# Kernel tuning notes

Hardware: AMD Instinct MI355X
Metric: run time of the kernel (lower is better)

Reference implementation:

```python
import jax, jax.numpy as jnp
import numpy as np

N_SEG = 64        # number of graphs in batch
NEG_SLOPE = 0.2   # PyG GATConv leaky_relu slope


def seg_softmax(vals, seg, num_segments):
    # vals: [E, H]; softmax over entries sharing the same segment id
    m = jax.ops.segment_max(vals, seg, num_segments=num_segments)
    m = jnp.where(jnp.isfinite(m), m, 0.0)  # guard empty segments
    e = jnp.exp(vals - m[seg])
    s = jax.ops.segment_sum(e, seg, num_segments=num_segments)
    return e / (s[seg] + 1e-16)


def setup_inputs() -> dict:
    key = jax.random.key(0)
    ks = jax.random.split(key, 16)
    N, E, Fin, H, C1, C2 = 50000, 800000, 128, 4, 32, 128
    x = jax.random.normal(ks[0], (N, Fin), jnp.float32)
    edge_index = jax.random.randint(ks[1], (2, E), 0, N)
    batch = jnp.sort(jax.random.randint(ks[2], (N,), 0, N_SEG))
    sc = lambda fan: 1.0 / np.sqrt(fan)
    W_gat = jax.random.normal(ks[3], (Fin, H * C1), jnp.float32) * sc(Fin)
    att_src = jax.random.normal(ks[4], (H, C1), jnp.float32) * sc(C1)
    att_dst = jax.random.normal(ks[5], (H, C1), jnp.float32) * sc(C1)
    b_gat = jnp.zeros((H * C1,), jnp.float32)
    bn1_w = jax.random.uniform(ks[6], (H * C1,), jnp.float32, 0.5, 1.5)
    bn1_b = jax.random.normal(ks[7], (H * C1,), jnp.float32) * 0.1
    W_gcn = jax.random.normal(ks[8], (H * C1, C2), jnp.float32) * sc(H * C1)
    b_gcn = jnp.zeros((C2,), jnp.float32)
    bn2_w = jax.random.uniform(ks[9], (C2,), jnp.float32, 0.5, 1.5)
    bn2_b = jax.random.normal(ks[10], (C2,), jnp.float32) * 0.1
    W_gate = jax.random.normal(ks[11], (C2, 1), jnp.float32) * sc(C2)
    b_gate = jnp.zeros((1,), jnp.float32)
    W_fc = jax.random.normal(ks[12], (C2, 1), jnp.float32) * sc(C2)
    b_fc = jnp.zeros((1,), jnp.float32)
    return dict(x=x, edge_index=edge_index, batch=batch, W_gat=W_gat,
                att_src=att_src, att_dst=att_dst, b_gat=b_gat,
                bn1_w=bn1_w, bn1_b=bn1_b, W_gcn=W_gcn, b_gcn=b_gcn,
                bn2_w=bn2_w, bn2_b=bn2_b, W_gate=W_gate, b_gate=b_gate,
                W_fc=W_fc, b_fc=b_fc)


def reference(x, edge_index, batch, W_gat, att_src, att_dst, b_gat,
              bn1_w, bn1_b, W_gcn, b_gcn, bn2_w, bn2_b,
              W_gate, b_gate, W_fc, b_fc):
    N = x.shape[0]
    H, C1 = att_src.shape
    loops = jnp.arange(N)
    src = jnp.concatenate([edge_index[0], loops])  # message source j
    dst = jnp.concatenate([edge_index[1], loops])  # aggregation target i

    # ---- GATConv (heads=4, concat, add_self_loops) ----
    h = (x @ W_gat).reshape(N, H, C1)                       # [N,H,C1]
    a_src = jnp.einsum('nhc,hc->nh', h, att_src)
    a_dst = jnp.einsum('nhc,hc->nh', h, att_dst)
    e = jax.nn.leaky_relu(a_src[src] + a_dst[dst], NEG_SLOPE)  # [E',H]
    alpha = seg_softmax(e, dst, N)
    msg = h[src] * alpha[..., None]                          # [E',H,C1]
    out1 = jax.ops.segment_sum(msg, dst, num_segments=N).reshape(N, H * C1) + b_gat
    out1 = jax.nn.elu(out1)
    out1 = out1 * bn1_w + bn1_b          # BatchNorm1d (eval: mean 0, var 1)
    # dropout: identity (eval mode)

    # ---- GCNConv (self-loops, symmetric normalization) ----
    deg = jax.ops.segment_sum(jnp.ones_like(dst, dtype=x.dtype), dst, num_segments=N)
    dinv = jax.lax.rsqrt(jnp.maximum(deg, 1.0))
    norm = dinv[src] * dinv[dst]                             # [E']
    h2 = out1 @ W_gcn                                        # [N,C2]
    out2 = jax.ops.segment_sum(h2[src] * norm[:, None], dst, num_segments=N) + b_gcn
    out2 = jax.nn.elu(out2)
    out2 = out2 * bn2_w + bn2_b

    # ---- GlobalAttention pooling ----
    gate = out2 @ W_gate + b_gate                            # [N,1]
    w = seg_softmax(gate, batch, N_SEG)
    graph_rep = jax.ops.segment_sum(w * out2, batch, num_segments=N_SEG)  # [G,C2]

    out = graph_rep @ W_fc + b_fc                            # [G,1]
    return out.squeeze(1)
```

## Files before the change

### kernel.cpp

```cpp
#include <hip/hip_runtime.h>
#include <math.h>


#define NEG_SLOPE 0.2f
#define BKT_BITS 7
#define BKT_SIZE 128
#define CHUNK_A 4096

typedef __attribute__((ext_vector_type(8))) short short8v;
typedef __attribute__((ext_vector_type(4))) float floatx4;

__device__ __forceinline__ int lower_bound_i(const int* a, int n, int key) {
    int lo = 0, hi = n;
    while (lo < hi) {
        int mid = (lo + hi) >> 1;
        if (a[mid] < key) lo = mid + 1; else hi = mid;
    }
    return lo;
}

__device__ __forceinline__ unsigned pack_bf16(float lo, float hi) {
    unsigned ua = __float_as_uint(lo);
    unsigned ub = __float_as_uint(hi);
    ua = ua + 0x7fffu + ((ua >> 16) & 1u);
    ub = ub + 0x7fffu + ((ub >> 16) & 1u);
    return (ua >> 16) | (ub & 0xffff0000u);
}

__device__ __forceinline__ unsigned short bf16_1(float v) {
    unsigned u = __float_as_uint(v);
    u = u + 0x7fffu + ((u >> 16) & 1u);
    return (unsigned short)(u >> 16);
}

__global__ __launch_bounds__(256) void k_front(
    const float* __restrict__ W1, const float* __restrict__ atts,
    const float* __restrict__ attd, const float* __restrict__ W2,
    unsigned short* __restrict__ Wf1, unsigned short* __restrict__ Wf2,
    const int* __restrict__ dst, int* __restrict__ bcount, int E, int NB)
{
    const int b = blockIdx.x;
    if (b < 2) {
        const int NCT = b ? 8 : 9;
        const float* W = b ? W2 : W1;
        unsigned short* Wf = b ? Wf2 : Wf1;
        const int lim = NCT * 4 * 64 * 8;
        for (int idx = threadIdx.x; idx < lim; idx += 256) {
            int j = idx & 7;
            int lane = (idx >> 3) & 63;
            int frag = idx >> 9;
            int ct = frag >> 2, ks = frag & 3;
            int quad = lane >> 4, l16 = lane & 15;
            int k = ks * 32 + quad * 8 + j;
            float v;
            if (ct < 8) {
                v = W[k * 128 + ct * 16 + l16];
            } else if (l16 < 4) {
                float s = 0.f;
                for (int c = 0; c < 32; c++) s += W1[k * 128 + l16 * 32 + c] * atts[l16 * 32 + c];
                v = s;
            } else if (l16 < 8) {
                int h = l16 - 4;
                float s = 0.f;
                for (int c = 0; c < 32; c++) s += W1[k * 128 + h * 32 + c] * attd[h * 32 + c];
                v = s;
            } else v = 0.f;
            Wf[idx] = bf16_1(v);
        }
    } else {
        __shared__ int h[512];
        const int tid = threadIdx.x;
        for (int i = tid; i < 512; i += 256) h[i] = 0;
        __syncthreads();
        int base = (b - 2) * 2048;
#pragma unroll
        for (int k = 0; k < 8; k++) {
            int e = base + k * 256 + tid;
            if (e < E) atomicAdd(&h[dst[e] >> BKT_BITS], 1);
        }
        __syncthreads();
        for (int i = tid; i < NB; i += 256) {
            int c = h[i];
            if (c) atomicAdd(&bcount[i], c);
        }
    }
}

template<int MODE>
__global__ __launch_bounds__(256) void k_gemm_mfma(
    const void* __restrict__ Ain, const unsigned short* __restrict__ Wf,
    unsigned* __restrict__ Cb, int N,
    const float* __restrict__ dinv,
    float* __restrict__ aS, float* __restrict__ aD)
{
    constexpr int NCT = (MODE == 0) ? 9 : 8;
    const int tid = threadIdx.x;
    const int wv = tid >> 6, lane = tid & 63;
    const int quad = lane >> 4, l16 = lane & 15;
    const int n0 = blockIdx.x * 64;
    const int arow = n0 + wv * 16 + l16;
    const bool rowok = arow < N;

    floatx4 acc[NCT];
#pragma unroll
    for (int ct = 0; ct < NCT; ct++) acc[ct] = (floatx4){0.f, 0.f, 0.f, 0.f};

    union AV { unsigned u[4]; short8v v; };

#pragma unroll
    for (int ks = 0; ks < 4; ks++) {
        AV a;
        a.u[0] = a.u[1] = a.u[2] = a.u[3] = 0u;
        if (rowok) {
            if (MODE == 0) {
                const float* A = (const float*)Ain;
                const float* p = A + (size_t)arow * 128 + ks * 32 + quad * 8;
                float4 va = *(const float4*)(p);
                float4 vb = *(const float4*)(p + 4);
                a.u[0] = pack_bf16(va.x, va.y);
                a.u[1] = pack_bf16(va.z, va.w);
                a.u[2] = pack_bf16(vb.x, vb.y);
                a.u[3] = pack_bf16(vb.z, vb.w);
            } else {
                const unsigned short* A = (const unsigned short*)Ain;
                a.v = *(const short8v*)(A + (size_t)arow * 128 + ks * 32 + quad * 8);
            }
        }
#pragma unroll
        for (int ct = 0; ct < NCT; ct++) {
            short8v bv = *(const short8v*)(Wf + ((ct * 4 + ks) << 9) + lane * 8);
            acc[ct] = __builtin_amdgcn_mfma_f32_16x16x32_bf16(a.v, bv, acc[ct], 0, 0, 0);
        }
    }

#pragma unroll
    for (int r = 0; r < 4; r++) {
        int n = n0 + wv * 16 + quad * 4 + r;
        if (n >= N) continue;
        float s = MODE ? dinv[n] : 1.f;
#pragma unroll
        for (int ct = 0; ct < 4; ct++) {
            Cb[(size_t)n * 64 + ct * 16 + l16] =
                pack_bf16(acc[ct][r] * s, acc[ct + 4][r] * s);
        }
        if (MODE == 0) {
            float e = acc[8][r];
            if (l16 < 4) aS[(size_t)n * 4 + l16] = e;
            else if (l16 < 8) aD[(size_t)n * 4 + (l16 - 4)] = e;
        }
    }
}

__global__ __launch_bounds__(512) void k_bscan(const int* __restrict__ bcount,
                                               int* __restrict__ bb,
                                               int* __restrict__ bcur, int NB)
{
    __shared__ int sc[512];
    const int tid = threadIdx.x;
    int own = (tid < NB) ? bcount[tid] : 0;
    sc[tid] = own;
    __syncthreads();
    for (int st = 1; st < 512; st <<= 1) {
        int v = 0;
        if (tid >= st) v = sc[tid - st];
        __syncthreads();
        if (tid >= st) sc[tid] += v;
        __syncthreads();
    }
    int excl = sc[tid] - own;
    if (tid < NB) { bb[tid] = excl; bcur[tid] = excl; }
    if (tid == 511) { bb[NB] = sc[511]; bcur[NB] = sc[511]; }
}

__global__ __launch_bounds__(256) void k_binA(const int* __restrict__ ei,
                                              int* __restrict__ bcur,
                                              int2* __restrict__ pairs,
                                              int E, int NB)
{
    __shared__ int h[512];
    __shared__ int base[512];
    const int tid = threadIdx.x;
    for (int i = tid; i < NB + 1; i += 256) h[i] = 0;
    __syncthreads();
    const int c0 = blockIdx.x * CHUNK_A;
    int s[16], d[16], b[16];
#pragma unroll
    for (int k = 0; k < 16; k++) {
        int e = c0 + k * 256 + tid;
        bool v = e < E;
        s[k] = v ? ei[e] : 0;
        d[k] = v ? ei[E + e] : 0;
        b[k] = v ? (d[k] >> BKT_BITS) : NB;
        atomicAdd(&h[b[k]], 1);
    }
    __syncthreads();
    for (int i = tid; i < NB + 1; i += 256) {
        int c = h[i];
        base[i] = c ? atomicAdd(&bcur[i], c) : 0;
        h[i] = 0;
    }
    __syncthreads();
#pragma unroll
    for (int k = 0; k < 16; k++) {
        int r = atomicAdd(&h[b[k]], 1);
        pairs[base[b[k]] + r] = make_int2(s[k], d[k]);
    }
}

__global__ __launch_bounds__(256) void k_binB(const int2* __restrict__ pairs,
                                              const int* __restrict__ bb,
                                              int* __restrict__ csr,
                                              int* __restrict__ offs,
                                              float* __restrict__ dinv,
                                              int N, int NB, int E)
{
    __shared__ int hist[BKT_SIZE], start[BKT_SIZE], cur[BKT_SIZE];
    __shared__ int sc[BKT_SIZE];
    const int tid = threadIdx.x;
    const int b = blockIdx.x;
    const int d0 = b << BKT_BITS;
    const int pbg = bb[b], peg = bb[b + 1];

    if (tid < BKT_SIZE) { hist[tid] = 0; cur[tid] = 0; }
    __syncthreads();
    for (int i = pbg + tid; i < peg; i += 256)
        atomicAdd(&hist[pairs[i].y - d0], 1);
    __syncthreads();
    int own = (tid < BKT_SIZE) ? hist[tid] : 0;
    if (tid < BKT_SIZE) sc[tid] = own;
    __syncthreads();
    for (int st = 1; st < BKT_SIZE; st <<= 1) {
        int v = 0;
        bool act = (tid < BKT_SIZE) && (tid >= st);
        if (act) v = sc[tid - st];
        __syncthreads();
        if (act) sc[tid] += v;
        __syncthreads();
    }
    if (tid < BKT_SIZE) {
        int abs0 = pbg + (sc[tid] - own);
        start[tid] = abs0;
        int d = d0 + tid;
        if (d < N) {
            offs[d] = abs0;
            dinv[d] = rsqrtf((float)(own + 1));
        }
    }
    if (tid == 0 && b == NB - 1) offs[N] = E;
    __syncthreads();
    for (int i = pbg + tid; i < peg; i += 256) {
        int2 p = pairs[i];
        int ld = p.y - d0;
        int r = atomicAdd(&cur[ld], 1);
        csr[start[ld] + r] = p.x;
    }
}

__global__ __launch_bounds__(256) void k_gat_aggr(
    const unsigned* __restrict__ hb, const float* __restrict__ aSg,
    const float* __restrict__ aDg, const int* __restrict__ offs,
    const int* __restrict__ csr,
    const float* __restrict__ bgat, const float* __restrict__ bn1w,
    const float* __restrict__ bn1b,
    unsigned short* __restrict__ raw1b, int N)
{
    __shared__ __align__(16) float s_u[4][64][4];
    __shared__ int s_s[4][64];

    const int wid = threadIdx.x >> 6;
    const int lane = threadIdx.x & 63;
    const int n = blockIdx.x * 4 + wid;
    if (n >= N) return;

    const int beg = offs[n];
    const int cnt = offs[n + 1] - beg + 1;
    const float4 ad = *(const float4*)(aDg + (size_t)n * 4);
    const int hA = lane >> 5;
    const float* pu = &s_u[wid][0][2 * hA];
    const int* ps = &s_s[wid][0];

    float t0 = 0.f, t1 = 0.f, t2 = 0.f, t3 = 0.f;
    float accLo = 0.f, accHi = 0.f;

    for (int base = 0; base < cnt; base += 64) {
        int idx = base + lane;
        bool valid = idx < cnt;
        int src = n;
        if (valid && idx > 0) src = csr[beg + idx - 1];
        float u0 = 0.f, u1 = 0.f, u2 = 0.f, u3 = 0.f;
        if (valid) {
            float4 as = *(const float4*)(aSg + (size_t)src * 4);
            float l0 = as.x + ad.x; l0 = (l0 > 0.f) ? l0 : NEG_SLOPE * l0;
            float l1 = as.y + ad.y; l1 = (l1 > 0.f) ? l1 : NEG_SLOPE * l1;
            float l2 = as.z + ad.z; l2 = (l2 > 0.f) ? l2 : NEG_SLOPE * l2;
            float l3 = as.w + ad.w; l3 = (l3 > 0.f) ? l3 : NEG_SLOPE * l3;
            u0 = __expf(l0); u1 = __expf(l1); u2 = __expf(l2); u3 = __expf(l3);
        }
        t0 += u0; t1 += u1; t2 += u2; t3 += u3;
        s_s[wid][lane] = src;
        *(float4*)&s_u[wid][lane][0] = make_float4(u0, u2, u1, u3);

        int cc = min(64, cnt - base);
        int j = 0;
        for (; j + 8 <= cc; j += 8) {
            int sj[8]; float2 uj[8]; unsigned vv[8];
#pragma unroll
            for (int k = 0; k < 8; k++) sj[k] = ps[j + k];
#pragma unroll
            for (int k = 0; k < 8; k++) uj[k] = *(const float2*)&pu[(j + k) * 4];
#pragma unroll
            for (int k = 0; k < 8; k++) vv[k] = hb[sj[k] * 64 + lane];
#pragma unroll
            for (int k = 0; k < 8; k++) {
                float lo = __uint_as_float(vv[k] << 16);
                float hi = __uint_as_float(vv[k] & 0xffff0000u);
                accLo += uj[k].x * lo;
                accHi += uj[k].y * hi;
            }
        }
        for (; j < cc; j++) {
            int sj = ps[j];
            float2 uv = *(const float2*)&pu[j * 4];
            unsigned v = hb[sj * 64 + lane];
            accLo += uv.x * __uint_as_float(v << 16);
            accHi += uv.y * __uint_as_float(v & 0xffff0000u);
        }
    }
#pragma unroll
    for (int msk = 1; msk < 64; msk <<= 1) {
        t0 += __shfl_xor(t0, msk);
        t1 += __shfl_xor(t1, msk);
        t2 += __shfl_xor(t2, msk);
        t3 += __shfl_xor(t3, msk);
    }
    float sLo = (hA ? t1 : t0) + 1e-16f;
    float sHi = (hA ? t3 : t2) + 1e-16f;
    float o0 = accLo / sLo + bgat[lane];
    o0 = (o0 > 0.f) ? o0 : expm1f(o0);
    o0 = o0 * bn1w[lane] + bn1b[lane];
    float o1 = accHi / sHi + bgat[lane + 64];
    o1 = (o1 > 0.f) ? o1 : expm1f(o1);
    o1 = o1 * bn1w[lane + 64] + bn1b[lane + 64];
    raw1b[(size_t)n * 128 + lane]      = bf16_1(o0);
    raw1b[(size_t)n * 128 + 64 + lane] = bf16_1(o1);
}

__global__ __launch_bounds__(256) void k_gcn_aggr(
    const unsigned* __restrict__ h2b, const int* __restrict__ offs,
    const int* __restrict__ csr, const float* __restrict__ dinv,
    const float* __restrict__ bgcn,
    const float* __restrict__ bn2w, const float* __restrict__ bn2b,
    const float* __restrict__ wgate, const float* __restrict__ bgate,
    const float* __restrict__ wfc,
    float* __restrict__ gate, float* __restrict__ fcdot, int N)
{
    __shared__ int s_s[4][64];

    const int wid = threadIdx.x >> 6;
    const int lane = threadIdx.x & 63;
    const int n = blockIdx.x * 4 + wid;
    if (n >= N) return;

    const int beg = offs[n];
    const int cnt = offs[n + 1] - beg + 1;
    const float dn = dinv[n];
    const int* ps = &s_s[wid][0];

    float accLo = 0.f, accHi = 0.f;
    for (int base = 0; base < cnt; base += 64) {
        int idx = base + lane;
        int src = n;
        if (idx > 0 && idx < cnt) src = csr[beg + idx - 1];
        s_s[wid][lane] = src;

        int cc = min(64, cnt - base);
        int j = 0;
        for (; j + 8 <= cc; j += 8) {
            int sj[8]; unsigned vv[8];
#pragma unroll
            for (int k = 0; k < 8; k++) sj[k] = ps[j + k];
#pragma unroll
            for (int k = 0; k < 8; k++) vv[k] = h2b[sj[k] * 64 + lane];
#pragma unroll
            for (int k = 0; k < 8; k++) {
                accLo += __uint_as_float(vv[k] << 16);
                accHi += __uint_as_float(vv[k] & 0xffff0000u);
            }
        }
        for (; j < cc; j++) {
            unsigned v = h2b[ps[j] * 64 + lane];
            accLo += __uint_as_float(v << 16);
            accHi += __uint_as_float(v & 0xffff0000u);
        }
    }
    float v0 = dn * accLo + bgcn[lane];
    v0 = (v0 > 0.f) ? v0 : expm1f(v0);
    v0 = v0 * bn2w[lane] + bn2b[lane];
    float v1 = dn * accHi + bgcn[lane + 64];
    v1 = (v1 > 0.f) ? v1 : expm1f(v1);
    v1 = v1 * bn2w[lane + 64] + bn2b[lane + 64];

    float g = v0 * wgate[lane] + v1 * wgate[lane + 64];
    float f = v0 * wfc[lane]   + v1 * wfc[lane + 64];
#pragma unroll
    for (int msk = 1; msk < 64; msk <<= 1) {
        g += __shfl_xor(g, msk);
        f += __shfl_xor(f, msk);
    }
    if (lane == 0) { gate[n] = g + bgate[0]; fcdot[n] = f; }
}

__global__ __launch_bounds__(256) void k_pool(
    const float* __restrict__ gate, const float* __restrict__ fcdot,
    const int* __restrict__ batch, const float* __restrict__ bfc,
    float* __restrict__ out, int N)
{
    __shared__ float red[256];
    __shared__ int range[2];
    const int g = blockIdx.x;
    const int tid = threadIdx.x;
    if (tid < 2) range[tid] = lower_bound_i(batch, N, g + tid);
    __syncthreads();
    const int lo = range[0], hi = range[1];
    float se = 0.f, sf = 0.f;
    for (int i = lo + tid; i < hi; i += 256) {
        float e = __expf(gate[i]);
        se += e;
        sf += e * fcdot[i];
    }
    red[tid] = se; __syncthreads();
    for (int s = 128; s > 0; s >>= 1) {
        if (tid < s) red[tid] += red[tid + s];
        __syncthreads();
    }
    se = red[0]; __syncthreads();
    red[tid] = sf; __syncthreads();
    for (int s = 128; s > 0; s >>= 1) {
        if (tid < s) red[tid] += red[tid + s];
        __syncthreads();
    }
    sf = red[0];
    if (tid == 0) out[g] = sf / (se + 1e-16f) + bfc[0];
}

extern "C" void kernel_launch(void* const* d_in, const int* in_sizes, int n_in,
                              void* d_out, int out_size, void* d_ws, size_t ws_size,
                              hipStream_t stream) {
    const float* x     = (const float*)d_in[0];
    const int*   ei    = (const int*)d_in[1];
    const int*   batch = (const int*)d_in[2];
    const float* Wgat  = (const float*)d_in[3];
    const float* atts  = (const float*)d_in[4];
    const float* attd  = (const float*)d_in[5];
    const float* bgat  = (const float*)d_in[6];
    const float* bn1w  = (const float*)d_in[7];
    const float* bn1b  = (const float*)d_in[8];
    const float* Wgcn  = (const float*)d_in[9];
    const float* bgcn  = (const float*)d_in[10];
    const float* bn2w  = (const float*)d_in[11];
    const float* bn2b  = (const float*)d_in[12];
    const float* wgate = (const float*)d_in[13];
    const float* bgate = (const float*)d_in[14];
    const float* wfc   = (const float*)d_in[15];
    const float* bfc   = (const float*)d_in[16];
    float* out = (float*)d_out;

    const int N = in_sizes[0] / 128;
    const int E = in_sizes[1] / 2;
    const int NB = (N + BKT_SIZE - 1) / BKT_SIZE;
    const int NHB = (E + 2047) / 2048;

    unsigned* hb  = (unsigned*)d_ws;
    unsigned* h2b = hb + (size_t)N * 64;
    unsigned short* raw1b = (unsigned short*)(h2b + (size_t)N * 64);
    int2* pairs  = (int2*)raw1b;
    float* aS    = (float*)(raw1b + (size_t)N * 128);
    float* aD    = aS + (size_t)N * 4;
    float* gate  = aD + (size_t)N * 4;
    float* fcdot = gate + N;
    float* dinv  = fcdot + N;
    int* offs   = (int*)(dinv + N);
    int* csr    = offs + (N + 1);
    int* bcount = csr + E;
    int* bb     = bcount + (NB + 1);
    int* bcur   = bb + (NB + 1);
    unsigned short* Wf1 = (unsigned short*)(bcur + (NB + 1));
    unsigned short* Wf2 = Wf1 + 9 * 4 * 64 * 8;

    hipMemsetAsync(bcount, 0, (size_t)(NB + 1) * sizeof(int), stream);

    const int gemm_blocks = (N + 63) / 64;
    const int aggr_blocks = (N + 3) / 4;

    k_front<<<NHB + 2, 256, 0, stream>>>(Wgat, atts, attd, Wgcn, Wf1, Wf2,
                                         ei + E, bcount, E, NB);
    k_gemm_mfma<0><<<gemm_blocks, 256, 0, stream>>>(x, Wf1, hb, N,
                                                    nullptr, aS, aD);
    k_bscan<<<1, 512, 0, stream>>>(bcount, bb, bcur, NB);
    k_binA<<<(E + CHUNK_A - 1) / CHUNK_A, 256, 0, stream>>>(ei, bcur, pairs, E, NB);
    k_binB<<<NB, 256, 0, stream>>>(pairs, bb, csr, offs, dinv, N, NB, E);
    k_gat_aggr<<<aggr_blocks, 256, 0, stream>>>(hb, aS, aD, offs, csr,
                                                bgat, bn1w, bn1b, raw1b, N);
    k_gemm_mfma<1><<<gemm_blocks, 256, 0, stream>>>(raw1b, Wf2, h2b, N,
                                                    dinv, nullptr, nullptr);
    k_gcn_aggr<<<aggr_blocks, 256, 0, stream>>>(h2b, offs, csr, dinv, bgcn,
                                                bn2w, bn2b, wgate, bgate, wfc,
                                                gate, fcdot, N);
    k_pool<<<64, 256, 0, stream>>>(gate, fcdot, batch, bfc, out, N);
}
```

Baseline: 270.7 us.

## Fuse bucket scan and binning into first GEMM launch as heterogeneous blocks

The separate bucket-scan kernel is removed. Each binning block and each binB block now redoes the 512-entry prefix scan over bucket counts in shared memory. The binning work is merged into the first MFMA GEMM launch, with block ranges split by index, so the two independent stages overlap and two launches go away. bcur now counts offsets relative to zero, so the memset is widened to cover it. In exchange, every block repeats the scan redundantly, and the design assumes NB is at most 511.

```diff
diff --git a/kernel.cpp b/kernel.cpp
--- a/kernel.cpp
+++ b/kernel.cpp
@@ -86,140 +86,135 @@
     }
 }
 
-template<int MODE>
-__global__ __launch_bounds__(256) void k_gemm_mfma(
-    const void* __restrict__ Ain, const unsigned short* __restrict__ Wf,
-    unsigned* __restrict__ Cb, int N,
-    const float* __restrict__ dinv,
-    float* __restrict__ aS, float* __restrict__ aD)
-{
-    constexpr int NCT = (MODE == 0) ? 9 : 8;
+__global__ __launch_bounds__(256) void k_gemm1_binA(
+    const float* __restrict__ x, const unsigned short* __restrict__ Wf1,
+    unsigned* __restrict__ hb, float* __restrict__ aS, float* __restrict__ aD,
+    const int* __restrict__ ei, const int* __restrict__ bcount,
+    int* __restrict__ bcur, int2* __restrict__ pairs,
+    int N, int E, int NB, int nGemm)
+{
     const int tid = threadIdx.x;
-    const int wv = tid >> 6, lane = tid & 63;
-    const int quad = lane >> 4, l16 = lane & 15;
-    const int n0 = blockIdx.x * 64;
-    const int arow = n0 + wv * 16 + l16;
-    const bool rowok = arow < N;
-
-    floatx4 acc[NCT];
-#pragma unroll
-    for (int ct = 0; ct < NCT; ct++) acc[ct] = (floatx4){0.f, 0.f, 0.f, 0.f};
-
-    union AV { unsigned u[4]; short8v v; };
-
-#pragma unroll
-    for (int ks = 0; ks < 4; ks++) {
-        AV a;
-        a.u[0] = a.u[1] = a.u[2] = a.u[3] = 0u;
-        if (rowok) {
-            if (MODE == 0) {
-                const float* A = (const float*)Ain;
-                const float* p = A + (size_t)arow * 128 + ks * 32 + quad * 8;
+    if ((int)blockIdx.x < nGemm) {
+        const int wv = tid >> 6, lane = tid & 63;
+        const int quad = lane >> 4, l16 = lane & 15;
+        const int n0 = blockIdx.x * 64;
+        const int arow = n0 + wv * 16 + l16;
+        const bool rowok = arow < N;
+
+        floatx4 acc[9];
+#pragma unroll
+        for (int ct = 0; ct < 9; ct++) acc[ct] = (floatx4){0.f, 0.f, 0.f, 0.f};
+        union AV { unsigned u[4]; short8v v; };
+#pragma unroll
+        for (int ks = 0; ks < 4; ks++) {
+            AV a;
+            a.u[0] = a.u[1] = a.u[2] = a.u[3] = 0u;
+            if (rowok) {
+                const float* p = x + (size_t)arow * 128 + ks * 32 + quad * 8;
                 float4 va = *(const float4*)(p);
                 float4 vb = *(const float4*)(p + 4);
                 a.u[0] = pack_bf16(va.x, va.y);
                 a.u[1] = pack_bf16(va.z, va.w);
                 a.u[2] = pack_bf16(vb.x, vb.y);
                 a.u[3] = pack_bf16(vb.z, vb.w);
-            } else {
-                const unsigned short* A = (const unsigned short*)Ain;
-                a.v = *(const short8v*)(A + (size_t)arow * 128 + ks * 32 + quad * 8);
             }
-        }
-#pragma unroll
-        for (int ct = 0; ct < NCT; ct++) {
-            short8v bv = *(const short8v*)(Wf + ((ct * 4 + ks) << 9) + lane * 8);
-            acc[ct] = __builtin_amdgcn_mfma_f32_16x16x32_bf16(a.v, bv, acc[ct], 0, 0, 0);
-        }
-    }
-
-#pragma unroll
-    for (int r = 0; r < 4; r++) {
-        int n = n0 + wv * 16 + quad * 4 + r;
-        if (n >= N) continue;
-        float s = MODE ? dinv[n] : 1.f;
-#pragma unroll
-        for (int ct = 0; ct < 4; ct++) {
-            Cb[(size_t)n * 64 + ct * 16 + l16] =
-                pack_bf16(acc[ct][r] * s, acc[ct + 4][r] * s);
-        }
-        if (MODE == 0) {
+#pragma unroll
+            for (int ct = 0; ct < 9; ct++) {
+                short8v bv = *(const short8v*)(Wf1 + ((ct * 4 + ks) << 9) + lane * 8);
+                acc[ct] = __builtin_amdgcn_mfma_f32_16x16x32_bf16(a.v, bv, acc[ct], 0, 0, 0);
+            }
+        }
+#pragma unroll
+        for (int r = 0; r < 4; r++) {
+            int n = n0 + wv * 16 + quad * 4 + r;
+            if (n >= N) continue;
+#pragma unroll
+            for (int ct = 0; ct < 4; ct++) {
+                hb[(size_t)n * 64 + ct * 16 + l16] =
+                    pack_bf16(acc[ct][r], acc[ct + 4][r]);
+            }
             float e = acc[8][r];
             if (l16 < 4) aS[(size_t)n * 4 + l16] = e;
             else if (l16 < 8) aD[(size_t)n * 4 + (l16 - 4)] = e;
         }
-    }
-}
-
-__global__ __launch_bounds__(512) void k_bscan(const int* __restrict__ bcount,
-                                               int* __restrict__ bb,
-                                               int* __restrict__ bcur, int NB)
-{
-    __shared__ int sc[512];
-    const int tid = threadIdx.x;
-    int own = (tid < NB) ? bcount[tid] : 0;
-    sc[tid] = own;
-    __syncthreads();
-    for (int st = 1; st < 512; st <<= 1) {
-        int v = 0;
-        if (tid >= st) v = sc[tid - st];
-        __syncthreads();
-        if (tid >= st) sc[tid] += v;
-        __syncthreads();
-    }
-    int excl = sc[tid] - own;
-    if (tid < NB) { bb[tid] = excl; bcur[tid] = excl; }
-    if (tid == 511) { bb[NB] = sc[511]; bcur[NB] = sc[511]; }
-}
-
-__global__ __launch_bounds__(256) void k_binA(const int* __restrict__ ei,
-                                              int* __restrict__ bcur,
-                                              int2* __restrict__ pairs,
-                                              int E, int NB)
-{
-    __shared__ int h[512];
-    __shared__ int base[512];
-    const int tid = threadIdx.x;
-    for (int i = tid; i < NB + 1; i += 256) h[i] = 0;
-    __syncthreads();
-    const int c0 = blockIdx.x * CHUNK_A;
-    int s[16], d[16], b[16];
-#pragma unroll
-    for (int k = 0; k < 16; k++) {
-        int e = c0 + k * 256 + tid;
-        bool v = e < E;
-        s[k] = v ? ei[e] : 0;
-        d[k] = v ? ei[E + e] : 0;
-        b[k] = v ? (d[k] >> BKT_BITS) : NB;
-        atomicAdd(&h[b[k]], 1);
-    }
-    __syncthreads();
-    for (int i = tid; i < NB + 1; i += 256) {
-        int c = h[i];
-        base[i] = c ? atomicAdd(&bcur[i], c) : 0;
-        h[i] = 0;
-    }
-    __syncthreads();
-#pragma unroll
-    for (int k = 0; k < 16; k++) {
-        int r = atomicAdd(&h[b[k]], 1);
-        pairs[base[b[k]] + r] = make_int2(s[k], d[k]);
+    } else {
+        __shared__ int sc[512];
+        __shared__ int bbloc[512];
+        __shared__ int h[512];
+        __shared__ int base[512];
+        const int chunk = blockIdx.x - nGemm;
+
+        const int p0 = tid, p1 = tid + 256;
+        int own0 = (p0 < NB) ? bcount[p0] : 0;
+        int own1 = (p1 < NB) ? bcount[p1] : 0;
+        sc[p0] = own0; sc[p1] = own1;
+        __syncthreads();
+        for (int st = 1; st < 512; st <<= 1) {
+            int r0 = (p0 >= st) ? sc[p0 - st] : 0;
+            int r1 = (p1 >= st) ? sc[p1 - st] : 0;
+            __syncthreads();
+            sc[p0] += r0; sc[p1] += r1;
+            __syncthreads();
+        }
+        bbloc[p0] = sc[p0] - own0;
+        bbloc[p1] = sc[p1] - own1;
+        h[p0] = 0; h[p1] = 0;
+        __syncthreads();
+
+        const int c0 = chunk * CHUNK_A;
+        int s[16], d[16], b[16];
+#pragma unroll
+        for (int k = 0; k < 16; k++) {
+            int e = c0 + k * 256 + tid;
+            bool v = e < E;
+            s[k] = v ? ei[e] : 0;
+            d[k] = v ? ei[E + e] : 0;
+            b[k] = v ? (d[k] >> BKT_BITS) : (NB < 511 ? 511 : NB);
+            atomicAdd(&h[b[k]], 1);
+        }
+        __syncthreads();
+        for (int i = tid; i < 512; i += 256) {
+            int c = h[i];
+            base[i] = (c && i < NB) ? (bbloc[i] + atomicAdd(&bcur[i], c)) : 0;
+            h[i] = 0;
+        }
+        __syncthreads();
+#pragma unroll
+        for (int k = 0; k < 16; k++) {
+            int r = atomicAdd(&h[b[k]], 1);
+            if (b[k] < NB) pairs[base[b[k]] + r] = make_int2(s[k], d[k]);
+        }
     }
 }
 
 __global__ __launch_bounds__(256) void k_binB(const int2* __restrict__ pairs,
-                                              const int* __restrict__ bb,
+                                              const int* __restrict__ bcount,
                                               int* __restrict__ csr,
                                               int* __restrict__ offs,
                                               float* __restrict__ dinv,
                                               int N, int NB, int E)
 {
+    __shared__ int scg[512];
     __shared__ int hist[BKT_SIZE], start[BKT_SIZE], cur[BKT_SIZE];
     __shared__ int sc[BKT_SIZE];
     const int tid = threadIdx.x;
     const int b = blockIdx.x;
     const int d0 = b << BKT_BITS;
-    const int pbg = bb[b], peg = bb[b + 1];
+
+    const int p0 = tid, p1 = tid + 256;
+    int own0 = (p0 < NB) ? bcount[p0] : 0;
+    int own1 = (p1 < NB) ? bcount[p1] : 0;
+    scg[p0] = own0; scg[p1] = own1;
+    __syncthreads();
+    for (int st = 1; st < 512; st <<= 1) {
+        int r0 = (p0 >= st) ? scg[p0 - st] : 0;
+        int r1 = (p1 >= st) ? scg[p1 - st] : 0;
+        __syncthreads();
+        scg[p0] += r0; scg[p1] += r1;
+        __syncthreads();
+    }
+    const int peg = scg[b];
+    const int pbg = peg - ((b < NB) ? bcount[b] : 0);
 
     if (tid < BKT_SIZE) { hist[tid] = 0; cur[tid] = 0; }
     __syncthreads();
@@ -343,6 +338,45 @@
     o1 = o1 * bn1w[lane + 64] + bn1b[lane + 64];
     raw1b[(size_t)n * 128 + lane]      = bf16_1(o0);
     raw1b[(size_t)n * 128 + 64 + lane] = bf16_1(o1);
+}
+
+__global__ __launch_bounds__(256) void k_gemm2(
+    const unsigned short* __restrict__ A, const unsigned short* __restrict__ Wf,
+    unsigned* __restrict__ Cb, int N, const float* __restrict__ dinv)
+{
+    const int tid = threadIdx.x;
+    const int wv = tid >> 6, lane = tid & 63;
+    const int quad = lane >> 4, l16 = lane & 15;
+    const int n0 = blockIdx.x * 64;
+    const int arow = n0 + wv * 16 + l16;
+    const bool rowok = arow < N;
+
+    floatx4 acc[8];
+#pragma unroll
+    for (int ct = 0; ct < 8; ct++) acc[ct] = (floatx4){0.f, 0.f, 0.f, 0.f};
+    union AV { unsigned u[4]; short8v v; };
+#pragma unroll
+    for (int ks = 0; ks < 4; ks++) {
+        AV a;
+        a.u[0] = a.u[1] = a.u[2] = a.u[3] = 0u;
+        if (rowok) a.v = *(const short8v*)(A + (size_t)arow * 128 + ks * 32 + quad * 8);
+#pragma unroll
+        for (int ct = 0; ct < 8; ct++) {
+            short8v bv = *(const short8v*)(Wf + ((ct * 4 + ks) << 9) + lane * 8);
+            acc[ct] = __builtin_amdgcn_mfma_f32_16x16x32_bf16(a.v, bv, acc[ct], 0, 0, 0);
+        }
+    }
+#pragma unroll
+    for (int r = 0; r < 4; r++) {
+        int n = n0 + wv * 16 + quad * 4 + r;
+        if (n >= N) continue;
+        float s = dinv[n];
+#pragma unroll
+        for (int ct = 0; ct < 4; ct++) {
+            Cb[(size_t)n * 64 + ct * 16 + l16] =
+                pack_bf16(acc[ct][r] * s, acc[ct + 4][r] * s);
+        }
+    }
 }
 
 __global__ __launch_bounds__(256) void k_gcn_aggr(
@@ -469,6 +503,7 @@
     const int E = in_sizes[1] / 2;
     const int NB = (N + BKT_SIZE - 1) / BKT_SIZE;
     const int NHB = (E + 2047) / 2048;
+    const int NCH = (E + CHUNK_A - 1) / CHUNK_A;
 
     unsigned* hb  = (unsigned*)d_ws;
     unsigned* h2b = hb + (size_t)N * 64;
@@ -482,27 +517,23 @@
     int* offs   = (int*)(dinv + N);
     int* csr    = offs + (N + 1);
     int* bcount = csr + E;
-    int* bb     = bcount + (NB + 1);
-    int* bcur   = bb + (NB + 1);
+    int* bcur   = bcount + (NB + 1);
     unsigned short* Wf1 = (unsigned short*)(bcur + (NB + 1));
     unsigned short* Wf2 = Wf1 + 9 * 4 * 64 * 8;
 
-    hipMemsetAsync(bcount, 0, (size_t)(NB + 1) * sizeof(int), stream);
+    hipMemsetAsync(bcount, 0, (size_t)(2 * (NB + 1)) * sizeof(int), stream);
 
     const int gemm_blocks = (N + 63) / 64;
     const int aggr_blocks = (N + 3) / 4;
 
     k_front<<<NHB + 2, 256, 0, stream>>>(Wgat, atts, attd, Wgcn, Wf1, Wf2,
                                          ei + E, bcount, E, NB);
-    k_gemm_mfma<0><<<gemm_blocks, 256, 0, stream>>>(x, Wf1, hb, N,
-                                                    nullptr, aS, aD);
-    k_bscan<<<1, 512, 0, stream>>>(bcount, bb, bcur, NB);
-    k_binA<<<(E + CHUNK_A - 1) / CHUNK_A, 256, 0, stream>>>(ei, bcur, pairs, E, NB);
-    k_binB<<<NB, 256, 0, stream>>>(pairs, bb, csr, offs, dinv, N, NB, E);
+    k_gemm1_binA<<<gemm_blocks + NCH, 256, 0, stream>>>(
+        x, Wf1, hb, aS, aD, ei, bcount, bcur, pairs, N, E, NB, gemm_blocks);
+    k_binB<<<NB, 256, 0, stream>>>(pairs, bcount, csr, offs, dinv, N, NB, E);
     k_gat_aggr<<<aggr_blocks, 256, 0, stream>>>(hb, aS, aD, offs, csr,
                                                 bgat, bn1w, bn1b, raw1b, N);
-    k_gemm_mfma<1><<<gemm_blocks, 256, 0, stream>>>(raw1b, Wf2, h2b, N,
-                                                    dinv, nullptr, nullptr);
+    k_gemm2<<<gemm_blocks, 256, 0, stream>>>(raw1b, Wf2, h2b, N, dinv);
     k_gcn_aggr<<<aggr_blocks, 256, 0, stream>>>(h2b, offs, csr, dinv, bgcn,
                                                 bn2w, bn2b, wgate, bgate, wfc,
                                                 gate, fcdot, N);
```

Measured after the change: 266.9 us. About the same (-1.4%).
